# Kernel tuning notes

Hardware: AMD Instinct MI355X
Metric: run time of the kernel (lower is better)

## Reference

```python
import jax, jax.numpy as jnp
import numpy as np

N = 50000      # nodes
E = 400000     # edges
F_IN = 128     # num_features
EMB = 64       # embedding_size
H1, H2, H3 = 4, 2, 1
G = 256        # number of graphs in batch
NEG_SLOPE = 0.2  # GATv2Conv default


def setup_inputs() -> dict:
    key = jax.random.key(0)
    ks = jax.random.split(key, 20)
    s = 0.1  # keep attention logits in a sane range
    return {
        "x": jax.random.normal(ks[0], (N, F_IN), dtype=jnp.float32),
        "edge_index": jax.random.randint(ks[1], (2, E), 0, N),
        "batch_index": jnp.sort(jax.random.randint(ks[2], (N,), 0, G)),
        "w1_l": jax.random.normal(ks[3], (H1 * EMB, F_IN), dtype=jnp.float32) * s,
        "w1_r": jax.random.normal(ks[4], (H1 * EMB, F_IN), dtype=jnp.float32) * s,
        "att1": jax.random.normal(ks[5], (H1, EMB), dtype=jnp.float32) * s,
        "b1": jax.random.normal(ks[6], (H1 * EMB,), dtype=jnp.float32) * s,
        "w2_l": jax.random.normal(ks[7], (H2 * EMB, H1 * EMB), dtype=jnp.float32) * s,
        "w2_r": jax.random.normal(ks[8], (H2 * EMB, H1 * EMB), dtype=jnp.float32) * s,
        "att2": jax.random.normal(ks[9], (H2, EMB), dtype=jnp.float32) * s,
        "b2": jax.random.normal(ks[10], (H2 * EMB,), dtype=jnp.float32) * s,
        "w3_l": jax.random.normal(ks[11], (H3 * EMB, H2 * EMB), dtype=jnp.float32) * s,
        "w3_r": jax.random.normal(ks[12], (H3 * EMB, H2 * EMB), dtype=jnp.float32) * s,
        "att3": jax.random.normal(ks[13], (H3, EMB), dtype=jnp.float32) * s,
        "b3": jax.random.normal(ks[14], (H3 * EMB,), dtype=jnp.float32) * s,
        "out_w": jax.random.normal(ks[15], (2, 2 * EMB), dtype=jnp.float32) * s,
        "out_b": jax.random.normal(ks[16], (2,), dtype=jnp.float32) * s,
    }


def gatv2_conv(x, src, dst, w_l, w_r, att, bias, heads):
    """PyG GATv2Conv (concat=True, add_self_loops already applied to src/dst)."""
    n = x.shape[0]
    d = att.shape[1]
    xl = (x @ w_l.T).reshape(n, heads, d)   # source transform
    xr = (x @ w_r.T).reshape(n, heads, d)   # target transform
    # per-edge attention logits: e_ij = att . leaky_relu(xl[j] + xr[i])
    z = jax.nn.leaky_relu(xl[src] + xr[dst], NEG_SLOPE)      # [E', H, D]
    e = jnp.einsum("ehd,hd->eh", z, att)                      # [E', H]
    # segment softmax over incoming edges of each target node
    m = jax.ops.segment_max(e, dst, num_segments=n)           # [N, H]
    p = jnp.exp(e - m[dst])
    ssum = jax.ops.segment_sum(p, dst, num_segments=n)        # [N, H]
    alpha = p / (ssum[dst] + 1e-16)
    out = jax.ops.segment_sum(alpha[:, :, None] * xl[src], dst, num_segments=n)
    return out.reshape(n, heads * d) + bias


def reference(x, edge_index, batch_index,
              w1_l, w1_r, att1, b1,
              w2_l, w2_r, att2, b2,
              w3_l, w3_r, att3, b3,
              out_w, out_b):
    n = x.shape[0]
    loop = jnp.arange(n, dtype=edge_index.dtype)
    src = jnp.concatenate([edge_index[0], loop])  # add self loops (PyG default)
    dst = jnp.concatenate([edge_index[1], loop])

    h = gatv2_conv(x, src, dst, w1_l, w1_r, att1, b1, H1)
    h = jax.nn.leaky_relu(h)  # slope 0.01 (F.leaky_relu default)
    h = gatv2_conv(h, src, dst, w2_l, w2_r, att2, b2, H2)
    h = jax.nn.leaky_relu(h)
    h = gatv2_conv(h, src, dst, w3_l, w3_r, att3, b3, H3)
    h = jax.nn.leaky_relu(h)

    # global max / mean pooling per graph
    gmax = jax.ops.segment_max(h, batch_index, num_segments=G)
    gsum = jax.ops.segment_sum(h, batch_index, num_segments=G)
    cnt = jax.ops.segment_sum(jnp.ones((n, 1), h.dtype), batch_index, num_segments=G)
    gmean = gsum / jnp.maximum(cnt, 1.0)
    hidden = jnp.concatenate([gmax, gmean], axis=1)           # [G, 2*EMB]
    out = hidden @ out_w.T + out_b                            # [G, 2]
    return (out, hidden)
```

## Files before the change

kernel.cpp:

```cpp
#include <hip/hip_runtime.h>
#include <hip/hip_bf16.h>
#include <cfloat>
#include <cstdint>


typedef __attribute__((ext_vector_type(8))) short bf16x8;
typedef __attribute__((ext_vector_type(4))) float f32x4;
typedef __attribute__((ext_vector_type(2))) float v2f;
typedef __attribute__((ext_vector_type(4))) unsigned short us4;
typedef __attribute__((ext_vector_type(2))) unsigned short us2;

#define L2E 1.4426950408889634f

__device__ __forceinline__ float bf2f(unsigned short u) {
    return __uint_as_float((unsigned)u << 16);
}
__device__ __forceinline__ unsigned short f2bf(float f) {
    unsigned u = __float_as_uint(f);
    u += 0x7FFFu + ((u >> 16) & 1u);
    return (unsigned short)(u >> 16);
}
__device__ __forceinline__ v2f unpack2(unsigned d) {
    v2f r;
    r.x = __uint_as_float(d << 16);
    r.y = __uint_as_float(d & 0xffff0000u);
    return r;
}
__device__ __forceinline__ unsigned pack2(float a, float b) {
    return (unsigned)f2bf(a) | ((unsigned)f2bf(b) << 16);
}

template<int CTRL>
__device__ __forceinline__ float dpp_add_f(float x) {
    int xi = __float_as_int(x);
    int yi = __builtin_amdgcn_update_dpp(xi, xi, CTRL, 0xF, 0xF, false);
    return x + __int_as_float(yi);
}
template<int PAT>
__device__ __forceinline__ float swz_add_f(float x) {
    int yi = __builtin_amdgcn_ds_swizzle(__float_as_int(x), PAT);
    return x + __int_as_float(yi);
}
template<int GS>
__device__ __forceinline__ float group_sum(float p) {
    p = dpp_add_f<0x121>(p);
    p = dpp_add_f<0x122>(p);
    p = dpp_add_f<0x124>(p);
    p = dpp_add_f<0x128>(p);
    if constexpr (GS >= 32) p = swz_add_f<0x401F>(p);
    if constexpr (GS >= 64) p += __shfl_xor(p, 32, 64);
    return p;
}

__global__ void init_k(int* __restrict__ deg, float* __restrict__ gsum,
                       float* __restrict__ gcnt, unsigned* __restrict__ gmaxu,
                       int N, int G)
{
    int i = blockIdx.x * blockDim.x + threadIdx.x;
    int stride = gridDim.x * blockDim.x;
    for (int k = i; k < N; k += stride) deg[k] = 0;
    for (int k = i; k < G * 64; k += stride) { gsum[k] = 0.f; gmaxu[k] = 0x00800000u; }
    for (int k = i; k < G; k += stride) gcnt[k] = 0.f;
}

__global__ void prep_k(const float* __restrict__ x, unsigned short* __restrict__ xb, int nx,
                       const float* p0, const float* p1, const float* p2,
                       const float* p3, const float* p4, const float* p5,
                       unsigned short* d0, unsigned short* d1, unsigned short* d2,
                       unsigned short* d3, unsigned short* d4, unsigned short* d5,
                       int s01, int s23, int s45,
                       const int* __restrict__ dste, int E, int N, int* __restrict__ deg)
{
    const int tid = blockIdx.x * blockDim.x + threadIdx.x;
    const int stride = gridDim.x * blockDim.x;

    for (int i = tid; i < nx / 4; i += stride) {
        int idx = i * 4;
        float4 v = *(const float4*)(x + idx);
        uint2 o = { pack2(v.x, v.y), pack2(v.z, v.w) };
        *(uint2*)(xb + idx) = o;
    }
    const int wtot4 = (2 * s01 + 2 * s23 + 2 * s45) / 4;
    const int t0 = 2 * s01, t1 = t0 + 2 * s23;
    for (int i = tid; i < wtot4; i += stride) {
        int e = i * 4;
        const float* s; unsigned short* d; int off;
        if (e < t0)      { int j = e;      s = (j < s01) ? p0 : p1; d = (j < s01) ? d0 : d1; off = j % s01; }
        else if (e < t1) { int j = e - t0; s = (j < s23) ? p2 : p3; d = (j < s23) ? d2 : d3; off = j % s23; }
        else             { int j = e - t1; s = (j < s45) ? p4 : p5; d = (j < s45) ? d4 : d5; off = j % s45; }
        float4 v = *(const float4*)(s + off);
        uint2 o = { pack2(v.x, v.y), pack2(v.z, v.w) };
        *(uint2*)(d + off) = o;
    }
    for (int e = tid; e < E + N; e += stride) {
        int i = (e < E) ? dste[e] : (e - E);
        atomicAdd(&deg[i], 1);
    }
}

template<int K, int SLAB>
__global__ __launch_bounds__(256) void gemm_lds(
    const unsigned short* __restrict__ A,
    const unsigned short* __restrict__ Wl, const unsigned short* __restrict__ Wr,
    unsigned short* __restrict__ Cl, unsigned short* __restrict__ Cr,
    int M, int Nout)
{
    constexpr int KC   = 128;
    constexpr int WPAD = KC + 8;
    constexpr int NT   = SLAB / 32;
    __shared__ unsigned short Ws[SLAB * WPAD];

    const int tid = threadIdx.x, wv = tid >> 6, lane = tid & 63;
    const int r16 = lane & 15, quad = lane >> 4;
    const int m0 = blockIdx.x * 64;
    const int mh = (wv >> 1) * 32;
    const int nh = (wv & 1) * (SLAB / 2);
    const int ncol0 = blockIdx.y * SLAB;

    f32x4 acc[2][2][NT] = {};

    const unsigned short* Arow[2];
    #pragma unroll
    for (int mt = 0; mt < 2; ++mt) {
        int r = m0 + mh + mt * 16 + r16;
        r = (r < M) ? r : (M - 1);
        Arow[mt] = A + (size_t)r * K + quad * 8;
    }

    for (int kc = 0; kc < K / KC; ++kc) {
        const int k0 = kc * KC;
        bf16x8 a[2][4];
        #pragma unroll
        for (int mt = 0; mt < 2; ++mt)
            #pragma unroll
            for (int ks = 0; ks < 4; ++ks)
                a[mt][ks] = *(const bf16x8*)(Arow[mt] + k0 + ks * 32);

        #pragma unroll
        for (int side = 0; side < 2; ++side) {
            const unsigned short* W = side ? Wr : Wl;
            __syncthreads();
            #pragma unroll
            for (int it = 0; it < SLAB * KC / 2048; ++it) {
                int idx8 = (it * 256 + tid) * 8;
                int row = idx8 >> 7, col = idx8 & 127;
                bf16x8 v = *(const bf16x8*)(W + (size_t)(ncol0 + row) * K + k0 + col);
                *(bf16x8*)(&Ws[row * WPAD + col]) = v;
            }
            __syncthreads();
            #pragma unroll
            for (int ks = 0; ks < 4; ++ks) {
                #pragma unroll
                for (int n = 0; n < NT; ++n) {
                    bf16x8 b = *(const bf16x8*)(&Ws[(nh + n * 16 + r16) * WPAD + ks * 32 + quad * 8]);
                    #pragma unroll
                    for (int mt = 0; mt < 2; ++mt)
                        acc[side][mt][n] = __builtin_amdgcn_mfma_f32_16x16x32_bf16(
                            a[mt][ks], b, acc[side][mt][n], 0, 0, 0);
                }
            }
        }
    }

    constexpr int RP  = SLAB / 2 + 8;
    constexpr int LPR = SLAB / 16;
    constexpr int RPI = 64 / LPR;
    const int il = lane % LPR, rr = lane / LPR;
    #pragma unroll
    for (int side = 0; side < 2; ++side) {
        unsigned short* C = side ? Cr : Cl;
        __syncthreads();
        unsigned short* L = &Ws[wv * 32 * RP];
        #pragma unroll
        for (int mt = 0; mt < 2; ++mt)
            #pragma unroll
            for (int n = 0; n < NT; ++n)
                #pragma unroll
                for (int r = 0; r < 4; ++r)
                    L[(mt * 16 + quad * 4 + r) * RP + n * 16 + r16] = f2bf(acc[side][mt][n][r]);
        #pragma unroll
        for (int t = 0; t < 32 / RPI; ++t) {
            int row = t * RPI + rr;
            uint4 v = *(const uint4*)(&L[row * RP + il * 8]);
            int gr = m0 + mh + row;
            if (gr < M)
                *(uint4*)(C + (size_t)gr * Nout + ncol0 + nh + il * 8) = v;
        }
    }
}

__global__ __launch_bounds__(1024) void scanA_k(const int* __restrict__ deg,
                                                int* __restrict__ rowptr,
                                                int* __restrict__ bsum, int N)
{
    __shared__ int parts[16];
    const int t = threadIdx.x, lane = t & 63, wv = t >> 6;
    const int base = blockIdx.x * 8192;
    int v[8];
    int run = 0;
    #pragma unroll
    for (int i = 0; i < 8; ++i) {
        int idx = base + t * 8 + i;
        run += (idx < N) ? deg[idx] : 0;
        v[i] = run;
    }
    int x = run;
    #pragma unroll
    for (int off = 1; off < 64; off <<= 1) {
        int y = __shfl_up(x, off, 64);
        if (lane >= off) x += y;
    }
    int excl = x - run;
    if (lane == 63) parts[wv] = x;
    __syncthreads();
    if (wv == 0 && lane < 16) {
        int p = parts[lane];
        int xx = p;
        #pragma unroll
        for (int off = 1; off < 16; off <<= 1) {
            int y = __shfl_up(xx, off, 64);
            if (lane >= off) xx += y;
        }
        parts[lane] = xx - p;
    }
    __syncthreads();
    int pre = parts[wv] + excl;
    #pragma unroll
    for (int i = 0; i < 8; ++i) {
        int idx = base + t * 8 + i;
        if (idx < N) rowptr[idx + 1] = pre + v[i];
    }
    if (t == 1023) bsum[blockIdx.x] = parts[15] + x;
}

__global__ void scanB_k(int* __restrict__ bsum, int B)
{
    int lane = threadIdx.x;
    int v = (lane < B) ? bsum[lane] : 0;
    int x = v;
    #pragma unroll
    for (int off = 1; off < 64; off <<= 1) {
        int y = __shfl_up(x, off, 64);
        if (lane >= off) x += y;
    }
    if (lane < B) bsum[lane] = x - v;
}

__global__ __launch_bounds__(1024) void scanC_k(int* __restrict__ rowptr,
                                                const int* __restrict__ bsum, int N)
{
    const int b = blockIdx.x, t = threadIdx.x;
    if (b == 0) { if (t == 0) rowptr[0] = 0; return; }
    const int off = bsum[b];
    const int base = b * 8192;
    #pragma unroll
    for (int i = 0; i < 8; ++i) {
        int idx = base + t * 8 + i;
        if (idx < N) rowptr[idx + 1] += off;
    }
}

__global__ void scatter_k(const int* __restrict__ src, const int* __restrict__ dst,
                          int E, int N, const int* __restrict__ rowptr,
                          int* __restrict__ deg, int* __restrict__ esrc)
{
    int e = blockIdx.x * blockDim.x + threadIdx.x;
    if (e >= E + N) return;
    int i = (e < E) ? dst[e] : (e - E);
    int j = (e < E) ? src[e] : (e - E);
    int old = atomicAdd(&deg[i], -1);
    esrc[rowptr[i] + old - 1] = j;
}

template<int P>
__device__ __forceinline__ float edge_logit(const v2f* xv, const v2f* xrv, const v2f* attv)
{
    v2f d = {0.f, 0.f};
    #pragma unroll
    for (int p = 0; p < P; ++p) {
        v2f z = xv[p] + xrv[p];
        v2f l = __builtin_elementwise_max(z, z * 0.2f);
        d += l * attv[p];
    }
    return d.x + d.y;
}

template<int P>
__device__ __forceinline__ void load_edge(const unsigned short* __restrict__ xl,
                                          size_t base, v2f* xv)
{
    if constexpr (P == 2) {
        uint2 a = *(const uint2*)(xl + base);
        xv[0] = unpack2(a.x); xv[1] = unpack2(a.y);
    } else {
        unsigned a = *(const unsigned*)(xl + base);
        xv[0] = unpack2(a);
    }
}

template<int H, bool BF16OUT>
__global__ __launch_bounds__(256) void fused_agg_k(
    const unsigned short* __restrict__ xl, const unsigned short* __restrict__ xr,
    const int* __restrict__ rowptr, const int* __restrict__ esrc,
    const float* __restrict__ att, const float* __restrict__ bias,
    void* __restrict__ outv, int N, float oslope)
{
    const int wid  = __builtin_amdgcn_readfirstlane(
                         (blockIdx.x * blockDim.x + threadIdx.x) >> 6);
    const int lane = threadIdx.x & 63;
    if (wid >= N) return;
    constexpr int HD = H * 64;
    constexpr int GS = 64 / H;
    const int f0 = lane * H;
    const int r0 = rowptr[wid];
    const int r1 = rowptr[wid + 1];

    if constexpr (H >= 2) {
        constexpr int P = H / 2;
        v2f xrv[P], attv[P], acc[P];
        load_edge<P>(xr, (size_t)wid * HD + f0, xrv);
        #pragma unroll
        for (int p = 0; p < P; ++p) {
            attv[p] = *(const v2f*)(att + f0 + 2 * p) * L2E;
            acc[p] = (v2f){0.f, 0.f};
        }

        float s = 0.f;
        int k = r0;
        for (; k + 4 <= r1; k += 4) {
            int j[4];
            #pragma unroll
            for (int i = 0; i < 4; ++i) j[i] = esrc[k + i];
            v2f xv[4][P];
            #pragma unroll
            for (int i = 0; i < 4; ++i)
                load_edge<P>(xl, (size_t)j[i] * HD + f0, xv[i]);
            float pl[4];
            #pragma unroll
            for (int i = 0; i < 4; ++i) pl[i] = edge_logit<P>(xv[i], xrv, attv);
            #pragma unroll
            for (int i = 0; i < 4; ++i) pl[i] = group_sum<GS>(pl[i]);
            float w[4];
            #pragma unroll
            for (int i = 0; i < 4; ++i) w[i] = __builtin_amdgcn_exp2f(pl[i]);
            s += (w[0] + w[1]) + (w[2] + w[3]);
            #pragma unroll
            for (int p = 0; p < P; ++p) {
                v2f t = xv[0][p] * w[0] + xv[1][p] * w[1];
                t += xv[2][p] * w[2] + xv[3][p] * w[3];
                acc[p] += t;
            }
        }
        for (; k < r1; ++k) {
            int j0 = esrc[k];
            v2f xv[P];
            load_edge<P>(xl, (size_t)j0 * HD + f0, xv);
            float pl = group_sum<GS>(edge_logit<P>(xv, xrv, attv));
            float w = __builtin_amdgcn_exp2f(pl);
            s += w;
            #pragma unroll
            for (int p = 0; p < P; ++p) acc[p] += xv[p] * w;
        }

        float rs = 1.f / (s + 1e-16f);
        unsigned short o[H];
        float of[H];
        #pragma unroll
        for (int p = 0; p < P; ++p) {
            v2f b2 = *(const v2f*)(bias + f0 + 2 * p);
            v2f v = acc[p] * rs + b2;
            v = __builtin_elementwise_max(v, v * oslope);
            if constexpr (BF16OUT) { o[2 * p] = f2bf(v.x); o[2 * p + 1] = f2bf(v.y); }
            else                   { of[2 * p] = v.x; of[2 * p + 1] = v.y; }
        }
        if constexpr (BF16OUT) {
            unsigned short* ou = (unsigned short*)outv;
            if constexpr (H == 4) *(us4*)(ou + (size_t)wid * HD + f0) = *(us4*)o;
            else                  *(us2*)(ou + (size_t)wid * HD + f0) = *(us2*)o;
        } else {
            float* off_ = (float*)outv;
            #pragma unroll
            for (int i = 0; i < H; ++i) off_[(size_t)wid * HD + f0 + i] = of[i];
        }
    } else {
        float xrv  = bf2f(xr[(size_t)wid * 64 + lane]);
        float attv = att[lane] * L2E;
        float s = 0.f, acc = 0.f;
        int k = r0;
        for (; k + 4 <= r1; k += 4) {
            int j[4];
            #pragma unroll
            for (int i = 0; i < 4; ++i) j[i] = esrc[k + i];
            float xv[4], pl[4], w[4];
            #pragma unroll
            for (int i = 0; i < 4; ++i) xv[i] = bf2f(xl[(size_t)j[i] * 64 + lane]);
            #pragma unroll
            for (int i = 0; i < 4; ++i) {
                float z = xv[i] + xrv;
                pl[i] = fmaxf(z, 0.2f * z) * attv;
            }
            #pragma unroll
            for (int i = 0; i < 4; ++i) pl[i] = group_sum<64>(pl[i]);
            #pragma unroll
            for (int i = 0; i < 4; ++i) w[i] = __builtin_amdgcn_exp2f(pl[i]);
            s += (w[0] + w[1]) + (w[2] + w[3]);
            acc += (xv[0] * w[0] + xv[1] * w[1]) + (xv[2] * w[2] + xv[3] * w[3]);
        }
        for (; k < r1; ++k) {
            float x0 = bf2f(xl[(size_t)esrc[k] * 64 + lane]);
            float z = x0 + xrv;
            float pl = group_sum<64>(fmaxf(z, 0.2f * z) * attv);
            float w = __builtin_amdgcn_exp2f(pl);
            s += w;
            acc += x0 * w;
        }
        float rs = 1.f / (s + 1e-16f);
        float v = acc * rs + bias[lane];
        v = fmaxf(v, oslope * v);
        if constexpr (BF16OUT)
            ((unsigned short*)outv)[(size_t)wid * 64 + lane] = f2bf(v);
        else
            ((float*)outv)[(size_t)wid * 64 + lane] = v;
    }
}

__device__ __forceinline__ unsigned fenc(float f) {
    unsigned u = __float_as_uint(f);
    return (u & 0x80000000u) ? ~u : (u | 0x80000000u);
}
__device__ __forceinline__ float fdec(unsigned u) {
    return __uint_as_float((u & 0x80000000u) ? (u & 0x7fffffffu) : ~u);
}

__global__ __launch_bounds__(256) void pool_k(
    const float* __restrict__ h, const int* __restrict__ batch, int N,
    unsigned* __restrict__ gmaxu, float* __restrict__ gsum, float* __restrict__ gcnt)
{
    const int wid  = (blockIdx.x * blockDim.x + threadIdx.x) >> 6;
    const int lane = threadIdx.x & 63;
    const int n0 = wid * 16;
    if (n0 >= N) return;
    int gcur = batch[n0];
    float vmax = -3.4e38f, vsum = 0.f;
    int cnt = 0;
    #pragma unroll 4
    for (int i = 0; i < 16; ++i) {
        int n = n0 + i;
        if (n >= N) break;
        int g = batch[n];
        if (g != gcur) {
            atomicMax(&gmaxu[gcur * 64 + lane], fenc(vmax));
            atomicAdd(&gsum[gcur * 64 + lane], vsum);
            if (lane == 0) atomicAdd(&gcnt[gcur], (float)cnt);
            gcur = g; vmax = -3.4e38f; vsum = 0.f; cnt = 0;
        }
        float v = h[(size_t)n * 64 + lane];
        vmax = fmaxf(vmax, v);
        vsum += v;
        cnt++;
    }
    atomicMax(&gmaxu[gcur * 64 + lane], fenc(vmax));
    atomicAdd(&gsum[gcur * 64 + lane], vsum);
    if (lane == 0) atomicAdd(&gcnt[gcur], (float)cnt);
}

__global__ __launch_bounds__(128) void final_k(
    const unsigned* __restrict__ gmaxu, const float* __restrict__ gsum,
    const float* __restrict__ gcnt, const float* __restrict__ out_w,
    const float* __restrict__ out_b, float* __restrict__ out,
    float* __restrict__ hid_out)
{
    const int g = blockIdx.x;
    const int t = threadIdx.x;
    __shared__ float hid[128];
    float v;
    if (t < 64) {
        v = fdec(gmaxu[g * 64 + t]);
    } else {
        float c = fmaxf(gcnt[g], 1.f);
        v = gsum[g * 64 + (t - 64)] / c;
    }
    hid[t] = v;
    hid_out[(size_t)g * 128 + t] = v;
    __syncthreads();
    const int w = t >> 6, lane = t & 63;
    float p = hid[lane] * out_w[w * 128 + lane] + hid[lane + 64] * out_w[w * 128 + 64 + lane];
    #pragma unroll
    for (int off = 32; off >= 1; off >>= 1) p += __shfl_xor(p, off, 64);
    if (lane == 0) out[g * 2 + w] = p + out_b[w];
}

extern "C" void kernel_launch(void* const* d_in, const int* in_sizes, int n_in,
                              void* d_out, int out_size, void* d_ws, size_t ws_size,
                              hipStream_t stream)
{
    const float* x    = (const float*)d_in[0];
    const int*   ei   = (const int*)d_in[1];
    const int*   batch= (const int*)d_in[2];
    const float* w1l  = (const float*)d_in[3];
    const float* w1r  = (const float*)d_in[4];
    const float* att1 = (const float*)d_in[5];
    const float* b1   = (const float*)d_in[6];
    const float* w2l  = (const float*)d_in[7];
    const float* w2r  = (const float*)d_in[8];
    const float* att2 = (const float*)d_in[9];
    const float* b2   = (const float*)d_in[10];
    const float* w3l  = (const float*)d_in[11];
    const float* w3r  = (const float*)d_in[12];
    const float* att3 = (const float*)d_in[13];
    const float* b3   = (const float*)d_in[14];
    const float* outw = (const float*)d_in[15];
    const float* outb = (const float*)d_in[16];

    const int N   = in_sizes[2];
    const int E   = in_sizes[1] / 2;
    const int E2  = E + N;
    const int G   = 256;
    const int FIN = in_sizes[0] / N;
    const int* src = ei;
    const int* dst = ei + E;

    char* ws = (char*)d_ws;
    size_t off = 0;
    auto alloc = [&](size_t bytes) -> void* {
        void* p = ws + off;
        off = (off + bytes + 255) & ~(size_t)255;
        return p;
    };
    unsigned short* xlb   = (unsigned short*)alloc((size_t)N * 256 * 2);
    unsigned short* xrb   = (unsigned short*)alloc((size_t)N * 256 * 2);
    unsigned short* xb    = (unsigned short*)alloc((size_t)N * 128 * 2);
    unsigned short* hAb   = (unsigned short*)alloc((size_t)N * 256 * 2);
    unsigned short* hBb   = (unsigned short*)alloc((size_t)N * 128 * 2);
    float*          h3    = (float*)alloc((size_t)N * 64 * 4);
    int*            rowptr= (int*)alloc((size_t)(N + 1) * 4);
    int*            deg   = (int*)alloc((size_t)N * 4);
    int*            esrc  = (int*)alloc((size_t)E2 * 4);
    int*            bsum  = (int*)alloc(64 * 4);
    unsigned*       gmaxu = (unsigned*)alloc((size_t)G * 64 * 4);
    float*          gsum  = (float*)alloc((size_t)G * 64 * 4);
    float*          gcnt  = (float*)alloc((size_t)G * 4);
    unsigned short* w1lb  = (unsigned short*)alloc(256 * 128 * 2);
    unsigned short* w1rb  = (unsigned short*)alloc(256 * 128 * 2);
    unsigned short* w2lb  = (unsigned short*)alloc(128 * 256 * 2);
    unsigned short* w2rb  = (unsigned short*)alloc(128 * 256 * 2);
    unsigned short* w3lb  = (unsigned short*)alloc(64 * 128 * 2);
    unsigned short* w3rb  = (unsigned short*)alloc(64 * 128 * 2);

    init_k<<<(N + 255) / 256, 256, 0, stream>>>(deg, gsum, gcnt, gmaxu, N, G);

    const int s1 = 256 * 128, s2 = 128 * 256, s3 = 64 * 128;
    prep_k<<<1024, 256, 0, stream>>>(x, xb, N * FIN,
        w1l, w1r, w2l, w2r, w3l, w3r, w1lb, w1rb, w2lb, w2rb, w3lb, w3rb,
        s1, s2, s3, dst, E, N, deg);

    const int nblk = (N + 8191) / 8192;
    scanA_k<<<nblk, 1024, 0, stream>>>(deg, rowptr, bsum, N);
    scanB_k<<<1, 64, 0, stream>>>(bsum, nblk);
    scanC_k<<<nblk, 1024, 0, stream>>>(rowptr, bsum, N);
    scatter_k<<<(E2 + 255) / 256, 256, 0, stream>>>(src, dst, E, N, rowptr, deg, esrc);

    const int gx  = (N + 63) / 64;
    const int nwb = (N * 64 + 255) / 256;

    gemm_lds<128, 128><<<dim3(gx, 2), 256, 0, stream>>>(
        xb, w1lb, w1rb, xlb, xrb, N, 256);
    fused_agg_k<4, true><<<nwb, 256, 0, stream>>>(xlb, xrb, rowptr, esrc, att1, b1, hAb, N, 0.01f);

    gemm_lds<256, 128><<<dim3(gx, 1), 256, 0, stream>>>(
        hAb, w2lb, w2rb, xlb, xrb, N, 128);
    fused_agg_k<2, true><<<nwb, 256, 0, stream>>>(xlb, xrb, rowptr, esrc, att2, b2, hBb, N, 0.01f);

    gemm_lds<128, 64><<<dim3(gx, 1), 256, 0, stream>>>(
        hBb, w3lb, w3rb, xlb, xrb, N, 64);
    fused_agg_k<1, false><<<nwb, 256, 0, stream>>>(xlb, xrb, rowptr, esrc, att3, b3, h3, N, 0.01f);

    const int pb = (N / 16 + 3) / 4;
    pool_k<<<pb, 256, 0, stream>>>(h3, batch, N, gmaxu, gsum, gcnt);
    final_k<<<G, 128, 0, stream>>>(gmaxu, gsum, gcnt, outw, outb,
                                   (float*)d_out, (float*)d_out + G * 2);
}
```

Before: 332.5 us.

## Merge CSR build and pooling tail into cooperative kernels; deepen edge unroll

Replaces the six launches for init, conversion, degree counting, three-stage scan and scatter with one cooperative kernel that separates phases with grid syncs. Pooling and the final linear layer are merged into a second cooperative kernel. The aggregation inner loop is refactored into a templated helper and gains an 8-edge unrolled path ahead of the 4-edge and scalar tails. This is meant to cut launch gaps and small-kernel overhead, at the cost of running the work on only 256 blocks, with a serial per-block prefix over block sums and grid-sync latency.

```diff
diff --git a/kernel.cpp b/kernel.cpp
--- a/kernel.cpp
+++ b/kernel.cpp
@@ -1,7 +1,10 @@
 #include <hip/hip_runtime.h>
+#include <hip/hip_cooperative_groups.h>
 #include <hip/hip_bf16.h>
 #include <cfloat>
 #include <cstdint>
+
+namespace cg = cooperative_groups;
 
 
 typedef __attribute__((ext_vector_type(8))) short bf16x8;
@@ -52,49 +55,112 @@
     return p;
 }
 
-__global__ void init_k(int* __restrict__ deg, float* __restrict__ gsum,
-                       float* __restrict__ gcnt, unsigned* __restrict__ gmaxu,
-                       int N, int G)
-{
-    int i = blockIdx.x * blockDim.x + threadIdx.x;
-    int stride = gridDim.x * blockDim.x;
-    for (int k = i; k < N; k += stride) deg[k] = 0;
-    for (int k = i; k < G * 64; k += stride) { gsum[k] = 0.f; gmaxu[k] = 0x00800000u; }
-    for (int k = i; k < G; k += stride) gcnt[k] = 0.f;
-}
-
-__global__ void prep_k(const float* __restrict__ x, unsigned short* __restrict__ xb, int nx,
-                       const float* p0, const float* p1, const float* p2,
-                       const float* p3, const float* p4, const float* p5,
-                       unsigned short* d0, unsigned short* d1, unsigned short* d2,
-                       unsigned short* d3, unsigned short* d4, unsigned short* d5,
-                       int s01, int s23, int s45,
-                       const int* __restrict__ dste, int E, int N, int* __restrict__ deg)
-{
+struct BuildArgs {
+    const float* x; unsigned short* xb; int nx;
+    const float* w0; const float* w1; const float* w2;
+    const float* w3; const float* w4; const float* w5;
+    unsigned short* d0; unsigned short* d1; unsigned short* d2;
+    unsigned short* d3; unsigned short* d4; unsigned short* d5;
+    int s01, s23, s45;
+    const int* src; const int* dst; int E; int N;
+    int* deg; int* rowptr; int* bsum; int* esrc;
+    float* gsum; float* gcnt; unsigned* gmaxu; int G;
+};
+
+__global__ __launch_bounds__(256) void build_k(BuildArgs a)
+{
+    cg::grid_group grid = cg::this_grid();
     const int tid = blockIdx.x * blockDim.x + threadIdx.x;
-    const int stride = gridDim.x * blockDim.x;
-
-    for (int i = tid; i < nx / 4; i += stride) {
+    const int gsz = gridDim.x * blockDim.x;
+
+    for (int k = tid; k < a.N; k += gsz) a.deg[k] = 0;
+    for (int k = tid; k < a.G * 64; k += gsz) { a.gsum[k] = 0.f; a.gmaxu[k] = 0x00800000u; }
+    for (int k = tid; k < a.G; k += gsz) a.gcnt[k] = 0.f;
+    for (int i = tid; i < a.nx / 4; i += gsz) {
         int idx = i * 4;
-        float4 v = *(const float4*)(x + idx);
+        float4 v = *(const float4*)(a.x + idx);
         uint2 o = { pack2(v.x, v.y), pack2(v.z, v.w) };
-        *(uint2*)(xb + idx) = o;
-    }
-    const int wtot4 = (2 * s01 + 2 * s23 + 2 * s45) / 4;
-    const int t0 = 2 * s01, t1 = t0 + 2 * s23;
-    for (int i = tid; i < wtot4; i += stride) {
-        int e = i * 4;
-        const float* s; unsigned short* d; int off;
-        if (e < t0)      { int j = e;      s = (j < s01) ? p0 : p1; d = (j < s01) ? d0 : d1; off = j % s01; }
-        else if (e < t1) { int j = e - t0; s = (j < s23) ? p2 : p3; d = (j < s23) ? d2 : d3; off = j % s23; }
-        else             { int j = e - t1; s = (j < s45) ? p4 : p5; d = (j < s45) ? d4 : d5; off = j % s45; }
-        float4 v = *(const float4*)(s + off);
-        uint2 o = { pack2(v.x, v.y), pack2(v.z, v.w) };
-        *(uint2*)(d + off) = o;
-    }
-    for (int e = tid; e < E + N; e += stride) {
-        int i = (e < E) ? dste[e] : (e - E);
-        atomicAdd(&deg[i], 1);
+        *(uint2*)(a.xb + idx) = o;
+    }
+    {
+        const int wtot4 = (2 * a.s01 + 2 * a.s23 + 2 * a.s45) / 4;
+        const int t0 = 2 * a.s01, t1 = t0 + 2 * a.s23;
+        for (int i = tid; i < wtot4; i += gsz) {
+            int e = i * 4;
+            const float* s; unsigned short* d; int off;
+            if (e < t0)      { int j = e;      s = (j < a.s01) ? a.w0 : a.w1; d = (j < a.s01) ? a.d0 : a.d1; off = j % a.s01; }
+            else if (e < t1) { int j = e - t0; s = (j < a.s23) ? a.w2 : a.w3; d = (j < a.s23) ? a.d2 : a.d3; off = j % a.s23; }
+            else             { int j = e - t1; s = (j < a.s45) ? a.w4 : a.w5; d = (j < a.s45) ? a.d4 : a.d5; off = j % a.s45; }
+            float4 v = *(const float4*)(s + off);
+            uint2 o = { pack2(v.x, v.y), pack2(v.z, v.w) };
+            *(uint2*)((unsigned short*)d + off) = o;
+        }
+    }
+    grid.sync();
+
+    for (int e = tid; e < a.E + a.N; e += gsz) {
+        int i = (e < a.E) ? a.dst[e] : (e - a.E);
+        atomicAdd(&a.deg[i], 1);
+    }
+    grid.sync();
+
+    const int nblk = (a.N + 8191) / 8192;
+    __shared__ int parts[4];
+    __shared__ int ptot;
+    if ((int)blockIdx.x < nblk) {
+        const int t = threadIdx.x, lane = t & 63, wv = t >> 6;
+        const int base = blockIdx.x * 8192;
+        int v[32];
+        int run = 0;
+        #pragma unroll
+        for (int i = 0; i < 32; ++i) {
+            int idx = base + t * 32 + i;
+            run += (idx < a.N) ? a.deg[idx] : 0;
+            v[i] = run;
+        }
+        int x = run;
+        #pragma unroll
+        for (int off = 1; off < 64; off <<= 1) {
+            int y = __shfl_up(x, off, 64);
+            if (lane >= off) x += y;
+        }
+        int excl = x - run;
+        if (lane == 63) parts[wv] = x;
+        __syncthreads();
+        if (t == 0) {
+            int acc2 = 0;
+            #pragma unroll
+            for (int w2 = 0; w2 < 4; ++w2) { int tmp = parts[w2]; parts[w2] = acc2; acc2 += tmp; }
+            ptot = acc2;
+        }
+        __syncthreads();
+        int pre = parts[wv] + excl;
+        #pragma unroll
+        for (int i = 0; i < 32; ++i) {
+            int idx = base + t * 32 + i;
+            if (idx < a.N) a.rowptr[idx + 1] = pre + v[i];
+        }
+        if (t == 0) a.bsum[blockIdx.x] = ptot;
+    }
+    grid.sync();
+
+    if ((int)blockIdx.x < nblk && blockIdx.x > 0) {
+        int off3 = 0;
+        for (int i = 0; i < (int)blockIdx.x; ++i) off3 += a.bsum[i];
+        const int base = blockIdx.x * 8192;
+        for (int i = threadIdx.x; i < 8192; i += 256) {
+            int idx = base + i;
+            if (idx < a.N) a.rowptr[idx + 1] += off3;
+        }
+    }
+    if (tid == 0) a.rowptr[0] = 0;
+    grid.sync();
+
+    for (int e = tid; e < a.E + a.N; e += gsz) {
+        int i = (e < a.E) ? a.dst[e] : (e - a.E);
+        int j = (e < a.E) ? a.src[e] : (e - a.E);
+        int old = atomicAdd(&a.deg[i], -1);
+        a.esrc[a.rowptr[i] + old - 1] = j;
     }
 }
 
@@ -189,89 +255,6 @@
     }
 }
 
-__global__ __launch_bounds__(1024) void scanA_k(const int* __restrict__ deg,
-                                                int* __restrict__ rowptr,
-                                                int* __restrict__ bsum, int N)
-{
-    __shared__ int parts[16];
-    const int t = threadIdx.x, lane = t & 63, wv = t >> 6;
-    const int base = blockIdx.x * 8192;
-    int v[8];
-    int run = 0;
-    #pragma unroll
-    for (int i = 0; i < 8; ++i) {
-        int idx = base + t * 8 + i;
-        run += (idx < N) ? deg[idx] : 0;
-        v[i] = run;
-    }
-    int x = run;
-    #pragma unroll
-    for (int off = 1; off < 64; off <<= 1) {
-        int y = __shfl_up(x, off, 64);
-        if (lane >= off) x += y;
-    }
-    int excl = x - run;
-    if (lane == 63) parts[wv] = x;
-    __syncthreads();
-    if (wv == 0 && lane < 16) {
-        int p = parts[lane];
-        int xx = p;
-        #pragma unroll
-        for (int off = 1; off < 16; off <<= 1) {
-            int y = __shfl_up(xx, off, 64);
-            if (lane >= off) xx += y;
-        }
-        parts[lane] = xx - p;
-    }
-    __syncthreads();
-    int pre = parts[wv] + excl;
-    #pragma unroll
-    for (int i = 0; i < 8; ++i) {
-        int idx = base + t * 8 + i;
-        if (idx < N) rowptr[idx + 1] = pre + v[i];
-    }
-    if (t == 1023) bsum[blockIdx.x] = parts[15] + x;
-}
-
-__global__ void scanB_k(int* __restrict__ bsum, int B)
-{
-    int lane = threadIdx.x;
-    int v = (lane < B) ? bsum[lane] : 0;
-    int x = v;
-    #pragma unroll
-    for (int off = 1; off < 64; off <<= 1) {
-        int y = __shfl_up(x, off, 64);
-        if (lane >= off) x += y;
-    }
-    if (lane < B) bsum[lane] = x - v;
-}
-
-__global__ __launch_bounds__(1024) void scanC_k(int* __restrict__ rowptr,
-                                                const int* __restrict__ bsum, int N)
-{
-    const int b = blockIdx.x, t = threadIdx.x;
-    if (b == 0) { if (t == 0) rowptr[0] = 0; return; }
-    const int off = bsum[b];
-    const int base = b * 8192;
-    #pragma unroll
-    for (int i = 0; i < 8; ++i) {
-        int idx = base + t * 8 + i;
-        if (idx < N) rowptr[idx + 1] += off;
-    }
-}
-
-__global__ void scatter_k(const int* __restrict__ src, const int* __restrict__ dst,
-                          int E, int N, const int* __restrict__ rowptr,
-                          int* __restrict__ deg, int* __restrict__ esrc)
-{
-    int e = blockIdx.x * blockDim.x + threadIdx.x;
-    if (e >= E + N) return;
-    int i = (e < E) ? dst[e] : (e - E);
-    int j = (e < E) ? src[e] : (e - E);
-    int old = atomicAdd(&deg[i], -1);
-    esrc[rowptr[i] + old - 1] = j;
-}
-
 template<int P>
 __device__ __forceinline__ float edge_logit(const v2f* xv, const v2f* xrv, const v2f* attv)
 {
@@ -298,6 +281,40 @@
     }
 }
 
+template<int U, int H>
+__device__ __forceinline__ void do_edges(
+    const unsigned short* __restrict__ xl, const int* __restrict__ esrc,
+    int k, int f0, const v2f* xrv, const v2f* attv, float& s, v2f* acc)
+{
+    constexpr int P  = H / 2;
+    constexpr int HD = H * 64;
+    constexpr int GS = 64 / H;
+    int j[U];
+    #pragma unroll
+    for (int i = 0; i < U; ++i) j[i] = esrc[k + i];
+    v2f xv[U][P];
+    #pragma unroll
+    for (int i = 0; i < U; ++i)
+        load_edge<P>(xl, (size_t)j[i] * HD + f0, xv[i]);
+    float pl[U];
+    #pragma unroll
+    for (int i = 0; i < U; ++i) pl[i] = edge_logit<P>(xv[i], xrv, attv);
+    #pragma unroll
+    for (int i = 0; i < U; ++i) pl[i] = group_sum<GS>(pl[i]);
+    float w[U];
+    #pragma unroll
+    for (int i = 0; i < U; ++i) w[i] = __builtin_amdgcn_exp2f(pl[i]);
+    #pragma unroll
+    for (int i = 0; i < U; ++i) s += w[i];
+    #pragma unroll
+    for (int p = 0; p < P; ++p) {
+        v2f t = {0.f, 0.f};
+        #pragma unroll
+        for (int i = 0; i < U; ++i) t += xv[i][p] * w[i];
+        acc[p] += t;
+    }
+}
+
 template<int H, bool BF16OUT>
 __global__ __launch_bounds__(256) void fused_agg_k(
     const unsigned short* __restrict__ xl, const unsigned short* __restrict__ xr,
@@ -310,7 +327,6 @@
     const int lane = threadIdx.x & 63;
     if (wid >= N) return;
     constexpr int HD = H * 64;
-    constexpr int GS = 64 / H;
     const int f0 = lane * H;
     const int r0 = rowptr[wid];
     const int r1 = rowptr[wid + 1];
@@ -327,40 +343,9 @@
 
         float s = 0.f;
         int k = r0;
-        for (; k + 4 <= r1; k += 4) {
-            int j[4];
-            #pragma unroll
-            for (int i = 0; i < 4; ++i) j[i] = esrc[k + i];
-            v2f xv[4][P];
-            #pragma unroll
-            for (int i = 0; i < 4; ++i)
-                load_edge<P>(xl, (size_t)j[i] * HD + f0, xv[i]);
-            float pl[4];
-            #pragma unroll
-            for (int i = 0; i < 4; ++i) pl[i] = edge_logit<P>(xv[i], xrv, attv);
-            #pragma unroll
-            for (int i = 0; i < 4; ++i) pl[i] = group_sum<GS>(pl[i]);
-            float w[4];
-            #pragma unroll
-            for (int i = 0; i < 4; ++i) w[i] = __builtin_amdgcn_exp2f(pl[i]);
-            s += (w[0] + w[1]) + (w[2] + w[3]);
-            #pragma unroll
-            for (int p = 0; p < P; ++p) {
-                v2f t = xv[0][p] * w[0] + xv[1][p] * w[1];
-                t += xv[2][p] * w[2] + xv[3][p] * w[3];
-                acc[p] += t;
-            }
-        }
-        for (; k < r1; ++k) {
-            int j0 = esrc[k];
-            v2f xv[P];
-            load_edge<P>(xl, (size_t)j0 * HD + f0, xv);
-            float pl = group_sum<GS>(edge_logit<P>(xv, xrv, attv));
-            float w = __builtin_amdgcn_exp2f(pl);
-            s += w;
-            #pragma unroll
-            for (int p = 0; p < P; ++p) acc[p] += xv[p] * w;
-        }
+        for (; k + 8 <= r1; k += 8) do_edges<8, H>(xl, esrc, k, f0, xrv, attv, s, acc);
+        for (; k + 4 <= r1; k += 4) do_edges<4, H>(xl, esrc, k, f0, xrv, attv, s, acc);
+        for (; k < r1; ++k)         do_edges<1, H>(xl, esrc, k, f0, xrv, attv, s, acc);
 
         float rs = 1.f / (s + 1e-16f);
         unsigned short o[H];
@@ -432,62 +417,68 @@
     return __uint_as_float((u & 0x80000000u) ? (u & 0x7fffffffu) : ~u);
 }
 
-__global__ __launch_bounds__(256) void pool_k(
-    const float* __restrict__ h, const int* __restrict__ batch, int N,
-    unsigned* __restrict__ gmaxu, float* __restrict__ gsum, float* __restrict__ gcnt)
-{
-    const int wid  = (blockIdx.x * blockDim.x + threadIdx.x) >> 6;
-    const int lane = threadIdx.x & 63;
-    const int n0 = wid * 16;
-    if (n0 >= N) return;
-    int gcur = batch[n0];
-    float vmax = -3.4e38f, vsum = 0.f;
-    int cnt = 0;
-    #pragma unroll 4
-    for (int i = 0; i < 16; ++i) {
-        int n = n0 + i;
-        if (n >= N) break;
-        int g = batch[n];
-        if (g != gcur) {
-            atomicMax(&gmaxu[gcur * 64 + lane], fenc(vmax));
-            atomicAdd(&gsum[gcur * 64 + lane], vsum);
-            if (lane == 0) atomicAdd(&gcnt[gcur], (float)cnt);
-            gcur = g; vmax = -3.4e38f; vsum = 0.f; cnt = 0;
-        }
-        float v = h[(size_t)n * 64 + lane];
-        vmax = fmaxf(vmax, v);
-        vsum += v;
-        cnt++;
-    }
-    atomicMax(&gmaxu[gcur * 64 + lane], fenc(vmax));
-    atomicAdd(&gsum[gcur * 64 + lane], vsum);
-    if (lane == 0) atomicAdd(&gcnt[gcur], (float)cnt);
-}
-
-__global__ __launch_bounds__(128) void final_k(
-    const unsigned* __restrict__ gmaxu, const float* __restrict__ gsum,
-    const float* __restrict__ gcnt, const float* __restrict__ out_w,
-    const float* __restrict__ out_b, float* __restrict__ out,
-    float* __restrict__ hid_out)
-{
+struct TailArgs {
+    const float* h3; const int* batch; int N;
+    unsigned* gmaxu; float* gsum; float* gcnt;
+    const float* outw; const float* outb;
+    float* out; float* hid_out; int G;
+};
+
+__global__ __launch_bounds__(256) void tail_k(TailArgs a)
+{
+    cg::grid_group grid = cg::this_grid();
+    const int wv = threadIdx.x >> 6, lane = threadIdx.x & 63;
+
+    const int nchunks = (a.N + 15) / 16;
+    for (int c = blockIdx.x * 4 + wv; c < nchunks; c += gridDim.x * 4) {
+        const int n0 = c * 16;
+        int gcur = a.batch[n0];
+        float vmax = -3.4e38f, vsum = 0.f;
+        int cnt = 0;
+        for (int i = 0; i < 16; ++i) {
+            int n = n0 + i;
+            if (n >= a.N) break;
+            int g = a.batch[n];
+            if (g != gcur) {
+                atomicMax(&a.gmaxu[gcur * 64 + lane], fenc(vmax));
+                atomicAdd(&a.gsum[gcur * 64 + lane], vsum);
+                if (lane == 0) atomicAdd(&a.gcnt[gcur], (float)cnt);
+                gcur = g; vmax = -3.4e38f; vsum = 0.f; cnt = 0;
+            }
+            float v = a.h3[(size_t)n * 64 + lane];
+            vmax = fmaxf(vmax, v);
+            vsum += v;
+            cnt++;
+        }
+        atomicMax(&a.gmaxu[gcur * 64 + lane], fenc(vmax));
+        atomicAdd(&a.gsum[gcur * 64 + lane], vsum);
+        if (lane == 0) atomicAdd(&a.gcnt[gcur], (float)cnt);
+    }
+    grid.sync();
+
     const int g = blockIdx.x;
     const int t = threadIdx.x;
     __shared__ float hid[128];
-    float v;
-    if (t < 64) {
-        v = fdec(gmaxu[g * 64 + t]);
-    } else {
-        float c = fmaxf(gcnt[g], 1.f);
-        v = gsum[g * 64 + (t - 64)] / c;
-    }
-    hid[t] = v;
-    hid_out[(size_t)g * 128 + t] = v;
-    __syncthreads();
-    const int w = t >> 6, lane = t & 63;
-    float p = hid[lane] * out_w[w * 128 + lane] + hid[lane + 64] * out_w[w * 128 + 64 + lane];
-    #pragma unroll
-    for (int off = 32; off >= 1; off >>= 1) p += __shfl_xor(p, off, 64);
-    if (lane == 0) out[g * 2 + w] = p + out_b[w];
+    if (g < a.G) {
+        if (t < 128) {
+            float v;
+            if (t < 64) v = fdec(a.gmaxu[g * 64 + t]);
+            else {
+                float c = fmaxf(a.gcnt[g], 1.f);
+                v = a.gsum[g * 64 + (t - 64)] / c;
+            }
+            hid[t] = v;
+            a.hid_out[(size_t)g * 128 + t] = v;
+        }
+        __syncthreads();
+        if (t < 128) {
+            const int w = t >> 6, ln = t & 63;
+            float p = hid[ln] * a.outw[w * 128 + ln] + hid[ln + 64] * a.outw[w * 128 + 64 + ln];
+            #pragma unroll
+            for (int off = 32; off >= 1; off >>= 1) p += __shfl_xor(p, off, 64);
+            if (ln == 0) a.out[g * 2 + w] = p + a.outb[w];
+        }
+    }
 }
 
 extern "C" void kernel_launch(void* const* d_in, const int* in_sizes, int n_in,
@@ -547,18 +538,16 @@
     unsigned short* w3lb  = (unsigned short*)alloc(64 * 128 * 2);
     unsigned short* w3rb  = (unsigned short*)alloc(64 * 128 * 2);
 
-    init_k<<<(N + 255) / 256, 256, 0, stream>>>(deg, gsum, gcnt, gmaxu, N, G);
-
-    const int s1 = 256 * 128, s2 = 128 * 256, s3 = 64 * 128;
-    prep_k<<<1024, 256, 0, stream>>>(x, xb, N * FIN,
-        w1l, w1r, w2l, w2r, w3l, w3r, w1lb, w1rb, w2lb, w2rb, w3lb, w3rb,
-        s1, s2, s3, dst, E, N, deg);
-
-    const int nblk = (N + 8191) / 8192;
-    scanA_k<<<nblk, 1024, 0, stream>>>(deg, rowptr, bsum, N);
-    scanB_k<<<1, 64, 0, stream>>>(bsum, nblk);
-    scanC_k<<<nblk, 1024, 0, stream>>>(rowptr, bsum, N);
-    scatter_k<<<(E2 + 255) / 256, 256, 0, stream>>>(src, dst, E, N, rowptr, deg, esrc);
+    BuildArgs ba;
+    ba.x = x; ba.xb = xb; ba.nx = N * FIN;
+    ba.w0 = w1l; ba.w1 = w1r; ba.w2 = w2l; ba.w3 = w2r; ba.w4 = w3l; ba.w5 = w3r;
+    ba.d0 = w1lb; ba.d1 = w1rb; ba.d2 = w2lb; ba.d3 = w2rb; ba.d4 = w3lb; ba.d5 = w3rb;
+    ba.s01 = 256 * 128; ba.s23 = 128 * 256; ba.s45 = 64 * 128;
+    ba.src = src; ba.dst = dst; ba.E = E; ba.N = N;
+    ba.deg = deg; ba.rowptr = rowptr; ba.bsum = bsum; ba.esrc = esrc;
+    ba.gsum = gsum; ba.gcnt = gcnt; ba.gmaxu = gmaxu; ba.G = G;
+    void* bargs[] = { &ba };
+    hipLaunchCooperativeKernel((void*)build_k, dim3(256), dim3(256), bargs, 0, stream);
 
     const int gx  = (N + 63) / 64;
     const int nwb = (N * 64 + 255) / 256;
@@ -575,8 +564,11 @@
         hBb, w3lb, w3rb, xlb, xrb, N, 64);
     fused_agg_k<1, false><<<nwb, 256, 0, stream>>>(xlb, xrb, rowptr, esrc, att3, b3, h3, N, 0.01f);
 
-    const int pb = (N / 16 + 3) / 4;
-    pool_k<<<pb, 256, 0, stream>>>(h3, batch, N, gmaxu, gsum, gcnt);
-    final_k<<<G, 128, 0, stream>>>(gmaxu, gsum, gcnt, outw, outb,
-                                   (float*)d_out, (float*)d_out + G * 2);
-}
+    TailArgs ta;
+    ta.h3 = h3; ta.batch = batch; ta.N = N;
+    ta.gmaxu = gmaxu; ta.gsum = gsum; ta.gcnt = gcnt;
+    ta.outw = outw; ta.outb = outb;
+    ta.out = (float*)d_out; ta.hid_out = (float*)d_out + G * 2; ta.G = G;
+    void* targs[] = { &ta };
+    hipLaunchCooperativeKernel((void*)tail_k, dim3(256), dim3(256), targs, 0, stream);
+}
```

Measured after the change: 548.9 us. +65.0%, slower.
